# Kernel tuning notes

Measured on AMD Instinct MI355X. Metric: run time of the kernel, lower is better.

The kernel has to match this reference:

```python
import jax, jax.numpy as jnp
import numpy as np

EPS = 1e-12  # F.normalize default eps


def setup_inputs() -> dict:
    key = jax.random.key(0)
    ks = jax.random.split(key, 8)
    b, c, h, w = 8, 192, 128, 128
    s = 0.02
    return {
        "x_in": jax.random.normal(ks[0], (b, c, h, w), dtype=jnp.float32),
        "w_split": jax.random.normal(ks[1], (c, c), dtype=jnp.float32) * s,
        "w_q": jax.random.normal(ks[2], (c, c), dtype=jnp.float32) * s,
        "w_k": jax.random.normal(ks[3], (c, c), dtype=jnp.float32) * s,
        "w_v": jax.random.normal(ks[4], (c, c), dtype=jnp.float32) * s,
        "w_proj": jax.random.normal(ks[5], (c, c), dtype=jnp.float32) * s,
        "b_proj": jax.random.normal(ks[6], (c,), dtype=jnp.float32) * s,
        "w_out": jax.random.normal(ks[7], (c, c), dtype=jnp.float32) * s,
    }


def _l2norm(x):
    # F.normalize(p=2, dim=-1): x / max(||x||, eps)
    n = jnp.sqrt(jnp.sum(x * x, axis=-1, keepdims=True))
    return x / jnp.maximum(n, EPS)


def reference(x_in, w_split, w_q, w_k, w_v, w_proj, b_proj, w_out):
    b, c, h, w = x_in.shape
    # conv_split0: 1x1 conv, no bias -> channel matmul
    x = jnp.einsum('oc,bchw->bohw', w_split, x_in)
    # [b,h,w,c] -> [b,hw,c]
    x = x.transpose(0, 2, 3, 1).reshape(b, h * w, c)
    # Linear: y = x @ W^T
    q = jnp.einsum('bnc,oc->bon', x, w_q)  # [b,c,hw] (already transposed)
    k = jnp.einsum('bnc,oc->bon', x, w_k)
    v = jnp.einsum('bnc,oc->bon', x, w_v)
    q = _l2norm(q)
    k = _l2norm(k)
    attn = jax.nn.softmax(jnp.einsum('bcn,bdn->bcd', k, q), axis=-1)  # [b,c,c]
    y = jnp.einsum('bcd,bdn->bcn', attn, v)  # [b,c,hw]
    y = y.transpose(0, 2, 1)  # [b,hw,c]
    out = jnp.einsum('bnc,oc->bno', y, w_proj) + b_proj
    out = out.reshape(b, h, w, c).transpose(0, 3, 1, 2)  # [b,c,h,w]
    out = jnp.einsum('oc,bchw->bohw', w_out, out)
    return out
```

## Files before the change

### kernel.cpp

```cpp
#include <hip/hip_runtime.h>


static constexpr int B_ = 8;
static constexpr int C_ = 192;
static constexpr int N_ = 16384;
static constexpr int CC2 = C_ * C_;
static constexpr int NCHUNK = 32;

using u16x8 = __attribute__((ext_vector_type(8))) unsigned short;
using bf16x8 = __attribute__((ext_vector_type(8))) __bf16;
using f32x4 = __attribute__((ext_vector_type(4))) float;
using uint32x4 = __attribute__((ext_vector_type(4))) unsigned int;

__device__ __forceinline__ unsigned short f2bf(float f) {
  unsigned int u = __builtin_bit_cast(unsigned int, f);
  u += 0x7FFFu + ((u >> 16) & 1u);
  return (unsigned short)(u >> 16);
}

__device__ __forceinline__ unsigned int pkbf(float lo, float hi) {
  unsigned short a = __builtin_bit_cast(unsigned short, (__bf16)lo);
  unsigned short b = __builtin_bit_cast(unsigned short, (__bf16)hi);
  return (unsigned int)a | ((unsigned int)b << 16);
}

__device__ __forceinline__ float f4get(const float4& v, int e) {
  return (e == 0) ? v.x : (e == 1) ? v.y : (e == 2) ? v.z : v.w;
}

__device__ __forceinline__ f32x4 mfma16(u16x8 a, u16x8 b, f32x4 c) {
  return __builtin_amdgcn_mfma_f32_16x16x32_bf16(
      __builtin_bit_cast(bf16x8, a), __builtin_bit_cast(bf16x8, b), c, 0, 0, 0);
}

__global__ void fold_kernel(const float* __restrict__ wsplit, const float* __restrict__ wq,
                            const float* __restrict__ wk, const float* __restrict__ wv,
                            const float* __restrict__ wproj, const float* __restrict__ bproj,
                            const float* __restrict__ wout,
                            float* __restrict__ Wq, float* __restrict__ WqT,
                            float* __restrict__ Wk, float* __restrict__ Wv,
                            float* __restrict__ Wo2, float* __restrict__ bias2) {
  int idx = blockIdx.x * 256 + threadIdx.x;
  if (idx < C_) {
    float s = 0.f;
    for (int c = 0; c < C_; ++c) s += wout[idx * C_ + c] * bproj[c];
    bias2[idx] = s;
  }
  if (idx >= 4 * CC2) return;
  int which = idx / CC2;
  int rem = idx % CC2;
  int o = rem / C_, c = rem % C_;
  const float* A = (which == 0) ? wq : (which == 1) ? wk : (which == 2) ? wv : wout;
  const float* Bm = (which == 3) ? wproj : wsplit;
  float s = 0.f;
  for (int e = 0; e < C_; ++e) s += A[o * C_ + e] * Bm[e * C_ + c];
  if (which == 0) { Wq[rem] = s; WqT[c * C_ + o] = s; }
  else if (which == 1) Wk[rem] = s;
  else if (which == 2) Wv[rem] = s;
  else Wo2[rem] = s;
}

template <bool ATOMIC>
__global__ __launch_bounds__(384) void gram3_kernel(const float* __restrict__ xin,
                                                    float* __restrict__ dst) {
  const int b = blockIdx.z, half = blockIdx.y, ch = blockIdx.x;
  const int k0 = ch * 512;
  __shared__ unsigned short Xs[2][C_][72];
  const int tid = threadIdx.x;
  const int wv = tid >> 6;
  const int lane = tid & 63;
  const int ln = lane & 15, mq = lane >> 4;
  const int arow0 = half * 96 + wv * 16;
  const int cbase = tid >> 4;
  const int k4 = tid & 15;
  const float* xb = xin + (size_t)b * C_ * N_;

  f32x4 acc[12];
#pragma unroll
  for (int j = 0; j < 12; ++j) acc[j] = (f32x4)0.0f;

  float4 ld[8];
  auto load_stage = [&](int kbase) {
#pragma unroll
    for (int j = 0; j < 8; ++j)
      ld[j] = *(const float4*)(xb + (size_t)(j * 24 + cbase) * N_ + kbase + k4 * 4);
  };
  auto write_stage = [&](int buf) {
#pragma unroll
    for (int j = 0; j < 8; ++j) {
      unsigned int lo = (unsigned)f2bf(ld[j].x) | ((unsigned)f2bf(ld[j].y) << 16);
      unsigned int hi = (unsigned)f2bf(ld[j].z) | ((unsigned)f2bf(ld[j].w) << 16);
      uint2 pk; pk.x = lo; pk.y = hi;
      *(uint2*)&Xs[buf][j * 24 + cbase][k4 * 4] = pk;
    }
  };

  load_stage(k0);
  write_stage(0);
  __syncthreads();
  for (int s = 0; s < 8; ++s) {
    if (s < 7) load_stage(k0 + (s + 1) * 64);
    const int cb = s & 1;
#pragma unroll
    for (int ks = 0; ks < 2; ++ks) {
      const int kk = ks * 32 + mq * 8;
      u16x8 a0 = *(const u16x8*)&Xs[cb][arow0 + ln][kk];
#pragma unroll
      for (int ct = 0; ct < 12; ++ct) {
        u16x8 bf = *(const u16x8*)&Xs[cb][ct * 16 + ln][kk];
        acc[ct] = mfma16(a0, bf, acc[ct]);
      }
    }
    if (s < 7) {
      write_stage(cb ^ 1);
      __syncthreads();
    }
  }
  float* out = ATOMIC ? dst + (size_t)b * CC2
                      : dst + ((size_t)b * NCHUNK + ch) * CC2;
#pragma unroll
  for (int ct = 0; ct < 12; ++ct)
#pragma unroll
    for (int r = 0; r < 4; ++r) {
      int row = arow0 + mq * 4 + r;
      int col = ct * 16 + ln;
      if (ATOMIC) atomicAdd(&out[row * C_ + col], acc[ct][r]);
      else out[row * C_ + col] = acc[ct][r];
    }
}

__global__ void gsum_kernel(const float* __restrict__ P, float* __restrict__ G) {
  const int j = (blockIdx.x * 256 + threadIdx.x) * 4;
  const int b = blockIdx.y;
  const float* base = P + (size_t)b * NCHUNK * CC2 + j;
  float4 s = {0.f, 0.f, 0.f, 0.f};
#pragma unroll
  for (int ch = 0; ch < NCHUNK; ++ch) {
    float4 v = *(const float4*)(base + (size_t)ch * CC2);
    s.x += v.x; s.y += v.y; s.z += v.z; s.w += v.w;
  }
  *(float4*)(G + (size_t)b * CC2 + j) = s;
}

__global__ __launch_bounds__(192) void tkqn_kernel(const float* __restrict__ Wk,
                                                   const float* __restrict__ Wq,
                                                   const float* __restrict__ G,
                                                   float* __restrict__ Tk,
                                                   float* __restrict__ qn) {
  const int b = blockIdx.y, d = blockIdx.x, t = threadIdx.x;
  const float* Gb = G + (size_t)b * CC2;
  float sk = 0.f, sq = 0.f;
  for (int c = 0; c < C_; ++c) {
    float g = Gb[c * C_ + t];
    sk += Wk[d * C_ + c] * g;
    sq += Wq[d * C_ + c] * g;
  }
  Tk[((size_t)b * C_ + d) * C_ + t] = sk;
  float val = sq * Wq[d * C_ + t];
  __shared__ float red[256];
  red[t] = val;
  if (t < 64) red[192 + t] = 0.f;
  __syncthreads();
  for (int st = 128; st > 0; st >>= 1) {
    if (t < st) red[t] += red[t + st];
    __syncthreads();
  }
  if (t == 0) qn[b * C_ + d] = fmaxf(sqrtf(fmaxf(red[0], 0.f)), 1e-12f);
}

__global__ __launch_bounds__(192) void attn_av_kernel(const float* __restrict__ Tk,
                                                      const float* __restrict__ WqT,
                                                      const float* __restrict__ Wk,
                                                      const float* __restrict__ Wv,
                                                      const float* __restrict__ qn,
                                                      float* __restrict__ Tv) {
  const int b = blockIdx.y, cc = blockIdx.x, t = threadIdx.x;
  __shared__ float tkrow[C_];
  __shared__ float arow[C_];
  __shared__ float red[256];
  tkrow[t] = Tk[((size_t)b * C_ + cc) * C_ + t];
  red[t] = tkrow[t] * Wk[cc * C_ + t];
  if (t < 64) red[192 + t] = 0.f;
  __syncthreads();
  for (int st = 128; st > 0; st >>= 1) {
    if (t < st) red[t] += red[t + st];
    __syncthreads();
  }
  float knv = fmaxf(sqrtf(fmaxf(red[0], 0.f)), 1e-12f);
  __syncthreads();
  float s = 0.f;
  for (int c = 0; c < C_; ++c) s += tkrow[c] * WqT[c * C_ + t];
  float lg = s / (knv * qn[b * C_ + t]);
  red[t] = lg;
  if (t < 64) red[192 + t] = -1e30f;
  __syncthreads();
  for (int st = 128; st > 0; st >>= 1) {
    if (t < st) red[t] = fmaxf(red[t], red[t + st]);
    __syncthreads();
  }
  float mx = red[0];
  __syncthreads();
  float e = expf(lg - mx);
  red[t] = e;
  if (t < 64) red[192 + t] = 0.f;
  __syncthreads();
  for (int st = 128; st > 0; st >>= 1) {
    if (t < st) red[t] += red[t + st];
    __syncthreads();
  }
  float a = e / red[0];
  arow[t] = a;
  __syncthreads();
  float sv = 0.f;
  for (int c = 0; c < C_; ++c) sv += arow[c] * Wv[c * C_ + t];
  Tv[((size_t)b * C_ + cc) * C_ + t] = sv;
}

__global__ void m_kernel(const float* __restrict__ Wo2, const float* __restrict__ Tv,
                         float* __restrict__ Mout) {
  int idx = blockIdx.x * 256 + threadIdx.x;
  if (idx >= B_ * CC2) return;
  int b = idx / CC2;
  int rc = idx % CC2;
  int i = rc / C_, j = rc % C_;
  float s = 0.f;
  for (int c = 0; c < C_; ++c) s += Wo2[i * C_ + c] * Tv[((size_t)b * C_ + c) * C_ + j];
  Mout[idx] = s;
}

__global__ __launch_bounds__(384, 4) void final3_kernel(const float* __restrict__ xin,
                                                        const float* __restrict__ Mw,
                                                        const float* __restrict__ bias2,
                                                        float* __restrict__ out) {
  const int b = blockIdx.y;
  const int p0 = blockIdx.x * 64;
  __shared__ __align__(16) unsigned short Ts[64 * 192];
  const int tid = threadIdx.x;
  const int wv = tid >> 6;
  const int lane = tid & 63;
  const int ln = lane & 15, mq = lane >> 4;
  const float* Mb = Mw + (size_t)b * CC2;

  const int c0 = (tid >> 3) * 4;
  const int pq = tid & 7;
  const float* xsrc = xin + ((size_t)b * C_ + c0) * N_ + p0 + pq * 4;

  float4 ldA[4], ldB[4];
#pragma unroll
  for (int l = 0; l < 4; ++l) ldA[l] = *(const float4*)(xsrc + (size_t)l * N_);

  u16x8 afr[6][2];
  float bo[2][4];
#pragma unroll
  for (int i = 0; i < 2; ++i) {
    int row = 32 * wv + 16 * i + ln;
#pragma unroll
    for (int kc = 0; kc < 6; ++kc) {
      const float* src = Mb + row * C_ + kc * 32 + mq * 8;
      float4 u0 = *(const float4*)(src);
      float4 u1 = *(const float4*)(src + 4);
      uint32x4 w;
      w[0] = pkbf(u0.x, u0.y); w[1] = pkbf(u0.z, u0.w);
      w[2] = pkbf(u1.x, u1.y); w[3] = pkbf(u1.z, u1.w);
      afr[kc][i] = __builtin_bit_cast(u16x8, w);
    }
#pragma unroll
    for (int r = 0; r < 4; ++r) bo[i][r] = bias2[32 * wv + 16 * i + mq * 4 + r];
  }

  auto stage_write = [&](const float4* ld, int sbase) {
#pragma unroll
    for (int e = 0; e < 4; ++e) {
      int p = sbase + pq * 4 + e;
      int idx = p * 192 + ((((c0 >> 3) ^ ((p >> 1) & 7)) << 3) | (c0 & 7));
      uint2 pk;
      pk.x = pkbf(f4get(ld[0], e), f4get(ld[1], e));
      pk.y = pkbf(f4get(ld[2], e), f4get(ld[3], e));
      *(uint2*)&Ts[idx] = pk;
    }
  };

  auto compute = [&](int pt) {
    const int p = pt * 16 + ln;
    const int pkey = (p >> 1) & 7;
    f32x4 acc0 = (f32x4)0.0f, acc1 = (f32x4)0.0f;
#pragma unroll
    for (int kc = 0; kc < 6; ++kc) {
      u16x8 bf = *(const u16x8*)&Ts[p * 192 + (((kc * 4 + mq) ^ pkey) << 3)];
      acc0 = mfma16(afr[kc][0], bf, acc0);
      acc1 = mfma16(afr[kc][1], bf, acc1);
    }
    const int pp = p0 + p;
#pragma unroll
    for (int r = 0; r < 4; ++r) {
      int row0 = 32 * wv + mq * 4 + r;
      out[((size_t)b * C_ + row0) * N_ + pp] = acc0[r] + bo[0][r];
      out[((size_t)b * C_ + row0 + 16) * N_ + pp] = acc1[r] + bo[1][r];
    }
  };

  stage_write(ldA, 0);
  __syncthreads();
#pragma unroll
  for (int l = 0; l < 4; ++l) ldB[l] = *(const float4*)(xsrc + 32 + (size_t)l * N_);
  compute(0);
  compute(1);
  stage_write(ldB, 32);
  __syncthreads();
  compute(2);
  compute(3);
}

extern "C" void kernel_launch(void* const* d_in, const int* in_sizes, int n_in,
                              void* d_out, int out_size, void* d_ws, size_t ws_size,
                              hipStream_t stream) {
  const float* xin    = (const float*)d_in[0];
  const float* wsplit = (const float*)d_in[1];
  const float* wq     = (const float*)d_in[2];
  const float* wk     = (const float*)d_in[3];
  const float* wv     = (const float*)d_in[4];
  const float* wproj  = (const float*)d_in[5];
  const float* bproj  = (const float*)d_in[6];
  const float* wout   = (const float*)d_in[7];
  float* out = (float*)d_out;

  float* ws = (float*)d_ws;
  float* G     = ws;
  float* Wq    = G + (size_t)B_ * CC2;
  float* WqT   = Wq + CC2;
  float* Wk    = WqT + CC2;
  float* Wv    = Wk + CC2;
  float* Wo2   = Wv + CC2;
  float* bias2 = Wo2 + CC2;
  float* Tk    = bias2 + 256;
  float* Tv    = Tk + (size_t)B_ * CC2;
  float* Mw    = Tv + (size_t)B_ * CC2;
  float* qn    = Mw + (size_t)B_ * CC2;
  float* P     = qn + 256 * B_;

  size_t base_floats = (size_t)(P - ws);
  size_t need_bytes = (base_floats + (size_t)B_ * NCHUNK * CC2) * sizeof(float);
  bool use_partials = ws_size >= need_bytes;

  fold_kernel<<<(4 * CC2 + 255) / 256, 256, 0, stream>>>(
      wsplit, wq, wk, wv, wproj, bproj, wout, Wq, WqT, Wk, Wv, Wo2, bias2);
  if (use_partials) {
    gram3_kernel<false><<<dim3(NCHUNK, 2, B_), 384, 0, stream>>>(xin, P);
    gsum_kernel<<<dim3(CC2 / 1024, B_), 256, 0, stream>>>(P, G);
  } else {
    hipMemsetAsync(G, 0, (size_t)B_ * CC2 * sizeof(float), stream);
    gram3_kernel<true><<<dim3(NCHUNK, 2, B_), 384, 0, stream>>>(xin, G);
  }
  tkqn_kernel<<<dim3(C_, B_), 192, 0, stream>>>(Wk, Wq, G, Tk, qn);
  attn_av_kernel<<<dim3(C_, B_), 192, 0, stream>>>(Tk, WqT, Wk, Wv, qn, Tv);
  m_kernel<<<(B_ * CC2 + 255) / 256, 256, 0, stream>>>(Wo2, Tv, Mw);
  final3_kernel<<<dim3(N_ / 64, B_), 384, 0, stream>>>(xin, Mw, bias2, out);
}
```

Before: 314.9 us.

## Fuse gram-reduction, attention and M-matrix kernels into one cooperative grid-synced kernel

Replaces the partial-sum, Tk/qn, attention/Tv and M-matrix kernels with one cooperative kernel of 512 blocks that separates phases with grid.sync. This removes three kernel launches and the gaps between them. In exchange each block processes three rows serially and grid-wide barriers are added. The bf16 packing in the gram kernel also switches to the native conversion.

```diff
diff --git a/kernel.cpp b/kernel.cpp
--- a/kernel.cpp
+++ b/kernel.cpp
@@ -1,4 +1,7 @@
 #include <hip/hip_runtime.h>
+#include <hip/hip_cooperative_groups.h>
+
+namespace cg = cooperative_groups;
 
 
 static constexpr int B_ = 8;
@@ -88,9 +91,9 @@
   auto write_stage = [&](int buf) {
 #pragma unroll
     for (int j = 0; j < 8; ++j) {
-      unsigned int lo = (unsigned)f2bf(ld[j].x) | ((unsigned)f2bf(ld[j].y) << 16);
-      unsigned int hi = (unsigned)f2bf(ld[j].z) | ((unsigned)f2bf(ld[j].w) << 16);
-      uint2 pk; pk.x = lo; pk.y = hi;
+      uint2 pk;
+      pk.x = pkbf(ld[j].x, ld[j].y);
+      pk.y = pkbf(ld[j].z, ld[j].w);
       *(uint2*)&Xs[buf][j * 24 + cbase][k4 * 4] = pk;
     }
   };
@@ -129,103 +132,122 @@
     }
 }
 
-__global__ void gsum_kernel(const float* __restrict__ P, float* __restrict__ G) {
-  const int j = (blockIdx.x * 256 + threadIdx.x) * 4;
-  const int b = blockIdx.y;
-  const float* base = P + (size_t)b * NCHUNK * CC2 + j;
-  float4 s = {0.f, 0.f, 0.f, 0.f};
-#pragma unroll
-  for (int ch = 0; ch < NCHUNK; ++ch) {
-    float4 v = *(const float4*)(base + (size_t)ch * CC2);
-    s.x += v.x; s.y += v.y; s.z += v.z; s.w += v.w;
-  }
-  *(float4*)(G + (size_t)b * CC2 + j) = s;
-}
-
-__global__ __launch_bounds__(192) void tkqn_kernel(const float* __restrict__ Wk,
-                                                   const float* __restrict__ Wq,
-                                                   const float* __restrict__ G,
-                                                   float* __restrict__ Tk,
-                                                   float* __restrict__ qn) {
-  const int b = blockIdx.y, d = blockIdx.x, t = threadIdx.x;
-  const float* Gb = G + (size_t)b * CC2;
-  float sk = 0.f, sq = 0.f;
-  for (int c = 0; c < C_; ++c) {
-    float g = Gb[c * C_ + t];
-    sk += Wk[d * C_ + c] * g;
-    sq += Wq[d * C_ + c] * g;
-  }
-  Tk[((size_t)b * C_ + d) * C_ + t] = sk;
-  float val = sq * Wq[d * C_ + t];
-  __shared__ float red[256];
-  red[t] = val;
-  if (t < 64) red[192 + t] = 0.f;
-  __syncthreads();
-  for (int st = 128; st > 0; st >>= 1) {
-    if (t < st) red[t] += red[t + st];
-    __syncthreads();
-  }
-  if (t == 0) qn[b * C_ + d] = fmaxf(sqrtf(fmaxf(red[0], 0.f)), 1e-12f);
-}
-
-__global__ __launch_bounds__(192) void attn_av_kernel(const float* __restrict__ Tk,
-                                                      const float* __restrict__ WqT,
-                                                      const float* __restrict__ Wk,
-                                                      const float* __restrict__ Wv,
-                                                      const float* __restrict__ qn,
-                                                      float* __restrict__ Tv) {
-  const int b = blockIdx.y, cc = blockIdx.x, t = threadIdx.x;
+template <bool SUMP>
+__global__ __launch_bounds__(256) void middle_kernel(
+    const float* __restrict__ P, float* __restrict__ G,
+    const float* __restrict__ Wk, const float* __restrict__ Wq,
+    const float* __restrict__ WqT, const float* __restrict__ Wv,
+    const float* __restrict__ Wo2, float* __restrict__ Tk,
+    float* __restrict__ qn, float* __restrict__ Tv, float* __restrict__ Mw) {
+  cg::grid_group grid = cg::this_grid();
+  const int blk = blockIdx.x;
+  const int t = threadIdx.x;
   __shared__ float tkrow[C_];
   __shared__ float arow[C_];
   __shared__ float red[256];
-  tkrow[t] = Tk[((size_t)b * C_ + cc) * C_ + t];
-  red[t] = tkrow[t] * Wk[cc * C_ + t];
-  if (t < 64) red[192 + t] = 0.f;
-  __syncthreads();
-  for (int st = 128; st > 0; st >>= 1) {
-    if (t < st) red[t] += red[t + st];
-    __syncthreads();
-  }
-  float knv = fmaxf(sqrtf(fmaxf(red[0], 0.f)), 1e-12f);
-  __syncthreads();
-  float s = 0.f;
-  for (int c = 0; c < C_; ++c) s += tkrow[c] * WqT[c * C_ + t];
-  float lg = s / (knv * qn[b * C_ + t]);
-  red[t] = lg;
-  if (t < 64) red[192 + t] = -1e30f;
-  __syncthreads();
-  for (int st = 128; st > 0; st >>= 1) {
-    if (t < st) red[t] = fmaxf(red[t], red[t + st]);
-    __syncthreads();
-  }
-  float mx = red[0];
-  __syncthreads();
-  float e = expf(lg - mx);
-  red[t] = e;
-  if (t < 64) red[192 + t] = 0.f;
-  __syncthreads();
-  for (int st = 128; st > 0; st >>= 1) {
-    if (t < st) red[t] += red[t + st];
-    __syncthreads();
-  }
-  float a = e / red[0];
-  arow[t] = a;
-  __syncthreads();
-  float sv = 0.f;
-  for (int c = 0; c < C_; ++c) sv += arow[c] * Wv[c * C_ + t];
-  Tv[((size_t)b * C_ + cc) * C_ + t] = sv;
-}
-
-__global__ void m_kernel(const float* __restrict__ Wo2, const float* __restrict__ Tv,
-                         float* __restrict__ Mout) {
-  int idx = blockIdx.x * 256 + threadIdx.x;
-  if (idx >= B_ * CC2) return;
-  int b = idx / CC2;
-  int rc = idx % CC2;
-  int i = rc / C_, j = rc % C_;
-  float s = 0.f;
-  for (int c = 0; c < C_; ++c) s += Wo2[i * C_ + c] * Tv[((size_t)b * C_ + c) * C_ + j];
-  Mout[idx] = s;
+
+  if (SUMP) {
+    for (int idx4 = blk * 256 + t; idx4 < B_ * CC2 / 4; idx4 += 512 * 256) {
+      int b = idx4 / (CC2 / 4);
+      int jj = idx4 % (CC2 / 4);
+      const float* base = P + (size_t)b * NCHUNK * CC2 + jj * 4;
+      float4 s = {0.f, 0.f, 0.f, 0.f};
+#pragma unroll
+      for (int ch = 0; ch < NCHUNK; ++ch) {
+        float4 v = *(const float4*)(base + (size_t)ch * CC2);
+        s.x += v.x; s.y += v.y; s.z += v.z; s.w += v.w;
+      }
+      *(float4*)(G + (size_t)b * CC2 + jj * 4) = s;
+    }
+    __threadfence();
+    grid.sync();
+  }
+
+  for (int r = 0; r < 3; ++r) {
+    const int task = blk + 512 * r;
+    const int b = task / C_, d = task % C_;
+    const float* Gb = G + (size_t)b * CC2;
+    float sq = 0.f;
+    if (t < C_) {
+      float sk = 0.f;
+      for (int c = 0; c < C_; ++c) {
+        float g = Gb[c * C_ + t];
+        sk += Wk[d * C_ + c] * g;
+        sq += Wq[d * C_ + c] * g;
+      }
+      Tk[((size_t)b * C_ + d) * C_ + t] = sk;
+    }
+    red[t] = (t < C_) ? sq * Wq[d * C_ + t] : 0.f;
+    __syncthreads();
+    for (int st = 128; st > 0; st >>= 1) {
+      if (t < st) red[t] += red[t + st];
+      __syncthreads();
+    }
+    if (t == 0) qn[b * C_ + d] = fmaxf(sqrtf(fmaxf(red[0], 0.f)), 1e-12f);
+    __syncthreads();
+  }
+  __threadfence();
+  grid.sync();
+
+  for (int r = 0; r < 3; ++r) {
+    const int task = blk + 512 * r;
+    const int b = task / C_, cc = task % C_;
+    float tkv = 0.f;
+    if (t < C_) {
+      tkv = Tk[((size_t)b * C_ + cc) * C_ + t];
+      tkrow[t] = tkv;
+    }
+    red[t] = (t < C_) ? tkv * Wk[cc * C_ + t] : 0.f;
+    __syncthreads();
+    for (int st = 128; st > 0; st >>= 1) {
+      if (t < st) red[t] += red[t + st];
+      __syncthreads();
+    }
+    float knv = fmaxf(sqrtf(fmaxf(red[0], 0.f)), 1e-12f);
+    __syncthreads();
+    float lg = -1e30f;
+    if (t < C_) {
+      float s = 0.f;
+      for (int c = 0; c < C_; ++c) s += tkrow[c] * WqT[c * C_ + t];
+      lg = s / (knv * qn[b * C_ + t]);
+    }
+    red[t] = lg;
+    __syncthreads();
+    for (int st = 128; st > 0; st >>= 1) {
+      if (t < st) red[t] = fmaxf(red[t], red[t + st]);
+      __syncthreads();
+    }
+    float mx = red[0];
+    __syncthreads();
+    float e = (t < C_) ? expf(lg - mx) : 0.f;
+    red[t] = e;
+    __syncthreads();
+    for (int st = 128; st > 0; st >>= 1) {
+      if (t < st) red[t] += red[t + st];
+      __syncthreads();
+    }
+    float a = e / red[0];
+    __syncthreads();
+    if (t < C_) arow[t] = a;
+    __syncthreads();
+    if (t < C_) {
+      float sv = 0.f;
+      for (int c = 0; c < C_; ++c) sv += arow[c] * Wv[c * C_ + t];
+      Tv[((size_t)b * C_ + cc) * C_ + t] = sv;
+    }
+    __syncthreads();
+  }
+  __threadfence();
+  grid.sync();
+
+  for (int idx = blk * 256 + t; idx < B_ * CC2; idx += 512 * 256) {
+    int b = idx / CC2;
+    int rc = idx % CC2;
+    int i = rc / C_, j = rc % C_;
+    float s = 0.f;
+    for (int c = 0; c < C_; ++c) s += Wo2[i * C_ + c] * Tv[((size_t)b * C_ + c) * C_ + j];
+    Mw[idx] = s;
+  }
 }
 
 __global__ __launch_bounds__(384, 4) void final3_kernel(const float* __restrict__ xin,
@@ -344,15 +366,25 @@
 
   fold_kernel<<<(4 * CC2 + 255) / 256, 256, 0, stream>>>(
       wsplit, wq, wk, wv, wproj, bproj, wout, Wq, WqT, Wk, Wv, Wo2, bias2);
+
   if (use_partials) {
     gram3_kernel<false><<<dim3(NCHUNK, 2, B_), 384, 0, stream>>>(xin, P);
-    gsum_kernel<<<dim3(CC2 / 1024, B_), 256, 0, stream>>>(P, G);
+    const float* Pc = P;
+    void* args[] = {(void*)&Pc, (void*)&G, (void*)&Wk, (void*)&Wq, (void*)&WqT,
+                    (void*)&Wv, (void*)&Wo2, (void*)&Tk, (void*)&qn, (void*)&Tv,
+                    (void*)&Mw};
+    hipLaunchCooperativeKernel((const void*)middle_kernel<true>, dim3(512), dim3(256),
+                               args, 0, stream);
   } else {
     hipMemsetAsync(G, 0, (size_t)B_ * CC2 * sizeof(float), stream);
     gram3_kernel<true><<<dim3(NCHUNK, 2, B_), 384, 0, stream>>>(xin, G);
-  }
-  tkqn_kernel<<<dim3(C_, B_), 192, 0, stream>>>(Wk, Wq, G, Tk, qn);
-  attn_av_kernel<<<dim3(C_, B_), 192, 0, stream>>>(Tk, WqT, Wk, Wv, qn, Tv);
-  m_kernel<<<(B_ * CC2 + 255) / 256, 256, 0, stream>>>(Wo2, Tv, Mw);
+    const float* Pc = G;
+    void* args[] = {(void*)&Pc, (void*)&G, (void*)&Wk, (void*)&Wq, (void*)&WqT,
+                    (void*)&Wv, (void*)&Wo2, (void*)&Tk, (void*)&qn, (void*)&Tv,
+                    (void*)&Mw};
+    hipLaunchCooperativeKernel((const void*)middle_kernel<false>, dim3(512), dim3(256),
+                               args, 0, stream);
+  }
+
   final3_kernel<<<dim3(N_ / 64, B_), 384, 0, stream>>>(xin, Mw, bias2, out);
 }
```

Measured after the change: 650.9 us. 2.07x slower.

## Rewrite small 192x192 attention-chain kernels with bf16 MFMA tiles

Applied to the files above, without the earlier changes.

Replaces the scalar per-row tkqn, attn_av and m kernels with MFMA-based tile kernels. Tk/norm, logits+softmax+AV, and the Wo2·Tv product each run as 16x16x32 bf16 MFMA GEMMs, with softmax reductions done via lane shuffles instead of shared-memory tree reductions. Tv is stored transposed in bf16 to feed the final GEMM directly. This adds bf16 rounding to small intermediate matrices, and the grids are now very small (24–48 blocks), which may underuse the GPU.

```diff
diff --git a/kernel.cpp b/kernel.cpp
--- a/kernel.cpp
+++ b/kernel.cpp
@@ -24,6 +24,15 @@
   return (unsigned int)a | ((unsigned int)b << 16);
 }
 
+__device__ __forceinline__ u16x8 ld8bf(const float* p) {
+  float4 u0 = *(const float4*)p;
+  float4 u1 = *(const float4*)(p + 4);
+  uint32x4 w;
+  w[0] = pkbf(u0.x, u0.y); w[1] = pkbf(u0.z, u0.w);
+  w[2] = pkbf(u1.x, u1.y); w[3] = pkbf(u1.z, u1.w);
+  return __builtin_bit_cast(u16x8, w);
+}
+
 __device__ __forceinline__ float f4get(const float4& v, int e) {
   return (e == 0) ? v.x : (e == 1) ? v.y : (e == 2) ? v.z : v.w;
 }
@@ -37,7 +46,7 @@
                             const float* __restrict__ wk, const float* __restrict__ wv,
                             const float* __restrict__ wproj, const float* __restrict__ bproj,
                             const float* __restrict__ wout,
-                            float* __restrict__ Wq, float* __restrict__ WqT,
+                            float* __restrict__ Wq, float* __restrict__ WvT,
                             float* __restrict__ Wk, float* __restrict__ Wv,
                             float* __restrict__ Wo2, float* __restrict__ bias2) {
   int idx = blockIdx.x * 256 + threadIdx.x;
@@ -54,9 +63,9 @@
   const float* Bm = (which == 3) ? wproj : wsplit;
   float s = 0.f;
   for (int e = 0; e < C_; ++e) s += A[o * C_ + e] * Bm[e * C_ + c];
-  if (which == 0) { Wq[rem] = s; WqT[c * C_ + o] = s; }
+  if (which == 0) Wq[rem] = s;
   else if (which == 1) Wk[rem] = s;
-  else if (which == 2) Wv[rem] = s;
+  else if (which == 2) { Wv[rem] = s; WvT[c * C_ + o] = s; }
   else Wo2[rem] = s;
 }
 
@@ -88,9 +97,9 @@
   auto write_stage = [&](int buf) {
 #pragma unroll
     for (int j = 0; j < 8; ++j) {
-      unsigned int lo = (unsigned)f2bf(ld[j].x) | ((unsigned)f2bf(ld[j].y) << 16);
-      unsigned int hi = (unsigned)f2bf(ld[j].z) | ((unsigned)f2bf(ld[j].w) << 16);
-      uint2 pk; pk.x = lo; pk.y = hi;
+      uint2 pk;
+      pk.x = pkbf(ld[j].x, ld[j].y);
+      pk.y = pkbf(ld[j].z, ld[j].w);
       *(uint2*)&Xs[buf][j * 24 + cbase][k4 * 4] = pk;
     }
   };
@@ -142,90 +151,175 @@
   *(float4*)(G + (size_t)b * CC2 + j) = s;
 }
 
-__global__ __launch_bounds__(192) void tkqn_kernel(const float* __restrict__ Wk,
-                                                   const float* __restrict__ Wq,
-                                                   const float* __restrict__ G,
-                                                   float* __restrict__ Tk,
-                                                   float* __restrict__ qn) {
-  const int b = blockIdx.y, d = blockIdx.x, t = threadIdx.x;
+__global__ __launch_bounds__(256) void tkqn2_kernel(
+    const float* __restrict__ Wk, const float* __restrict__ Wq,
+    const float* __restrict__ G, float* __restrict__ Tk,
+    float* __restrict__ kn, float* __restrict__ qn) {
+  const int b = blockIdx.y;
+  const int row0 = blockIdx.x * 64;
+  const int tid = threadIdx.x;
+  const int w = tid >> 6, lane = tid & 63;
+  const int ln = lane & 15, mq = lane >> 4;
+  const int rbase = row0 + w * 16;
+  const bool isq = rbase >= C_;
+  const float* W2 = isq ? Wq : Wk;
+  const int rloc = isq ? rbase - C_ : rbase;
   const float* Gb = G + (size_t)b * CC2;
-  float sk = 0.f, sq = 0.f;
-  for (int c = 0; c < C_; ++c) {
-    float g = Gb[c * C_ + t];
-    sk += Wk[d * C_ + c] * g;
-    sq += Wq[d * C_ + c] * g;
-  }
-  Tk[((size_t)b * C_ + d) * C_ + t] = sk;
-  float val = sq * Wq[d * C_ + t];
-  __shared__ float red[256];
-  red[t] = val;
-  if (t < 64) red[192 + t] = 0.f;
+
+  f32x4 acc[12];
+#pragma unroll
+  for (int j = 0; j < 12; ++j) acc[j] = (f32x4)0.0f;
+
+  for (int kc = 0; kc < 6; ++kc) {
+    u16x8 a = ld8bf(W2 + (size_t)(rloc + ln) * C_ + kc * 32 + mq * 8);
+#pragma unroll
+    for (int ct = 0; ct < 12; ++ct) {
+      u16x8 g = ld8bf(Gb + (size_t)(ct * 16 + ln) * C_ + kc * 32 + mq * 8);
+      acc[ct] = mfma16(a, g, acc[ct]);
+    }
+  }
+  const float* wr = W2 + (size_t)(rloc + mq * 4) * C_;
+  float nrm[4] = {0.f, 0.f, 0.f, 0.f};
+#pragma unroll
+  for (int ct = 0; ct < 12; ++ct)
+#pragma unroll
+    for (int r = 0; r < 4; ++r)
+      nrm[r] += acc[ct][r] * wr[r * C_ + ct * 16 + ln];
+#pragma unroll
+  for (int m = 1; m < 16; m <<= 1)
+#pragma unroll
+    for (int r = 0; r < 4; ++r) nrm[r] += __shfl_xor(nrm[r], m);
+  if (ln == 0) {
+#pragma unroll
+    for (int r = 0; r < 4; ++r) {
+      float v = fmaxf(sqrtf(fmaxf(nrm[r], 0.f)), 1e-12f);
+      int row = rbase + mq * 4 + r;
+      if (row < C_) kn[b * 256 + row] = v;
+      else qn[b * 256 + row - C_] = v;
+    }
+  }
+  if (!isq) {
+#pragma unroll
+    for (int ct = 0; ct < 12; ++ct)
+#pragma unroll
+      for (int r = 0; r < 4; ++r)
+        Tk[((size_t)b * C_ + rbase + mq * 4 + r) * C_ + ct * 16 + ln] = acc[ct][r];
+  }
+}
+
+__global__ __launch_bounds__(256) void attn2_kernel(
+    const float* __restrict__ Tk, const float* __restrict__ Wq,
+    const float* __restrict__ WvT, const float* __restrict__ kn,
+    const float* __restrict__ qn, unsigned short* __restrict__ Tvt) {
+  __shared__ unsigned short As[64 * 200];
+  const int b = blockIdx.y;
+  const int row0 = blockIdx.x * 64;
+  const int tid = threadIdx.x;
+  const int w = tid >> 6, lane = tid & 63;
+  const int ln = lane & 15, mq = lane >> 4;
+  const int rbase = row0 + w * 16;
+
+  f32x4 acc[12];
+#pragma unroll
+  for (int j = 0; j < 12; ++j) acc[j] = (f32x4)0.0f;
+  for (int kc = 0; kc < 6; ++kc) {
+    u16x8 a = ld8bf(Tk + ((size_t)b * C_ + rbase + ln) * C_ + kc * 32 + mq * 8);
+#pragma unroll
+    for (int ct = 0; ct < 12; ++ct) {
+      u16x8 q = ld8bf(Wq + (size_t)(ct * 16 + ln) * C_ + kc * 32 + mq * 8);
+      acc[ct] = mfma16(a, q, acc[ct]);
+    }
+  }
+  float rkn[4], rqn[12];
+#pragma unroll
+  for (int r = 0; r < 4; ++r) rkn[r] = kn[b * 256 + rbase + mq * 4 + r];
+#pragma unroll
+  for (int ct = 0; ct < 12; ++ct) rqn[ct] = qn[b * 256 + ct * 16 + ln];
+
+  float mx[4] = {-1e30f, -1e30f, -1e30f, -1e30f};
+#pragma unroll
+  for (int ct = 0; ct < 12; ++ct)
+#pragma unroll
+    for (int r = 0; r < 4; ++r) {
+      float l = acc[ct][r] / (rkn[r] * rqn[ct]);
+      acc[ct][r] = l;
+      mx[r] = fmaxf(mx[r], l);
+    }
+#pragma unroll
+  for (int m = 1; m < 16; m <<= 1)
+#pragma unroll
+    for (int r = 0; r < 4; ++r) mx[r] = fmaxf(mx[r], __shfl_xor(mx[r], m));
+  float sm[4] = {0.f, 0.f, 0.f, 0.f};
+#pragma unroll
+  for (int ct = 0; ct < 12; ++ct)
+#pragma unroll
+    for (int r = 0; r < 4; ++r) {
+      float e = expf(acc[ct][r] - mx[r]);
+      acc[ct][r] = e;
+      sm[r] += e;
+    }
+#pragma unroll
+  for (int m = 1; m < 16; m <<= 1)
+#pragma unroll
+    for (int r = 0; r < 4; ++r) sm[r] += __shfl_xor(sm[r], m);
+  float inv[4];
+#pragma unroll
+  for (int r = 0; r < 4; ++r) inv[r] = 1.f / sm[r];
+#pragma unroll
+  for (int ct = 0; ct < 12; ++ct)
+#pragma unroll
+    for (int r = 0; r < 4; ++r) {
+      int lrow = w * 16 + mq * 4 + r;
+      As[lrow * 200 + ct * 16 + ln] = f2bf(acc[ct][r] * inv[r]);
+    }
   __syncthreads();
-  for (int st = 128; st > 0; st >>= 1) {
-    if (t < st) red[t] += red[t + st];
-    __syncthreads();
-  }
-  if (t == 0) qn[b * C_ + d] = fmaxf(sqrtf(fmaxf(red[0], 0.f)), 1e-12f);
-}
-
-__global__ __launch_bounds__(192) void attn_av_kernel(const float* __restrict__ Tk,
-                                                      const float* __restrict__ WqT,
-                                                      const float* __restrict__ Wk,
-                                                      const float* __restrict__ Wv,
-                                                      const float* __restrict__ qn,
-                                                      float* __restrict__ Tv) {
-  const int b = blockIdx.y, cc = blockIdx.x, t = threadIdx.x;
-  __shared__ float tkrow[C_];
-  __shared__ float arow[C_];
-  __shared__ float red[256];
-  tkrow[t] = Tk[((size_t)b * C_ + cc) * C_ + t];
-  red[t] = tkrow[t] * Wk[cc * C_ + t];
-  if (t < 64) red[192 + t] = 0.f;
-  __syncthreads();
-  for (int st = 128; st > 0; st >>= 1) {
-    if (t < st) red[t] += red[t + st];
-    __syncthreads();
-  }
-  float knv = fmaxf(sqrtf(fmaxf(red[0], 0.f)), 1e-12f);
-  __syncthreads();
-  float s = 0.f;
-  for (int c = 0; c < C_; ++c) s += tkrow[c] * WqT[c * C_ + t];
-  float lg = s / (knv * qn[b * C_ + t]);
-  red[t] = lg;
-  if (t < 64) red[192 + t] = -1e30f;
-  __syncthreads();
-  for (int st = 128; st > 0; st >>= 1) {
-    if (t < st) red[t] = fmaxf(red[t], red[t + st]);
-    __syncthreads();
-  }
-  float mx = red[0];
-  __syncthreads();
-  float e = expf(lg - mx);
-  red[t] = e;
-  if (t < 64) red[192 + t] = 0.f;
-  __syncthreads();
-  for (int st = 128; st > 0; st >>= 1) {
-    if (t < st) red[t] += red[t + st];
-    __syncthreads();
-  }
-  float a = e / red[0];
-  arow[t] = a;
-  __syncthreads();
-  float sv = 0.f;
-  for (int c = 0; c < C_; ++c) sv += arow[c] * Wv[c * C_ + t];
-  Tv[((size_t)b * C_ + cc) * C_ + t] = sv;
-}
-
-__global__ void m_kernel(const float* __restrict__ Wo2, const float* __restrict__ Tv,
-                         float* __restrict__ Mout) {
-  int idx = blockIdx.x * 256 + threadIdx.x;
-  if (idx >= B_ * CC2) return;
-  int b = idx / CC2;
-  int rc = idx % CC2;
-  int i = rc / C_, j = rc % C_;
-  float s = 0.f;
-  for (int c = 0; c < C_; ++c) s += Wo2[i * C_ + c] * Tv[((size_t)b * C_ + c) * C_ + j];
-  Mout[idx] = s;
+
+  f32x4 tv[12];
+#pragma unroll
+  for (int j = 0; j < 12; ++j) tv[j] = (f32x4)0.0f;
+  for (int kc = 0; kc < 6; ++kc) {
+    u16x8 a2 = *(const u16x8*)&As[(w * 16 + ln) * 200 + kc * 32 + mq * 8];
+#pragma unroll
+    for (int ct = 0; ct < 12; ++ct) {
+      u16x8 q = ld8bf(WvT + (size_t)(ct * 16 + ln) * C_ + kc * 32 + mq * 8);
+      tv[ct] = mfma16(a2, q, tv[ct]);
+    }
+  }
+#pragma unroll
+  for (int ct = 0; ct < 12; ++ct) {
+    uint2 pk;
+    pk.x = pkbf(tv[ct][0], tv[ct][1]);
+    pk.y = pkbf(tv[ct][2], tv[ct][3]);
+    *(uint2*)&Tvt[((size_t)b * C_ + ct * 16 + ln) * C_ + row0 + w * 16 + mq * 4] = pk;
+  }
+}
+
+__global__ __launch_bounds__(256) void m2_kernel(
+    const float* __restrict__ Wo2, const unsigned short* __restrict__ Tvt,
+    float* __restrict__ Mw) {
+  const int b = blockIdx.y;
+  const int row0 = blockIdx.x * 64;
+  const int tid = threadIdx.x;
+  const int w = tid >> 6, lane = tid & 63;
+  const int ln = lane & 15, mq = lane >> 4;
+  const int rbase = row0 + w * 16;
+
+  f32x4 acc[12];
+#pragma unroll
+  for (int j = 0; j < 12; ++j) acc[j] = (f32x4)0.0f;
+  for (int kc = 0; kc < 6; ++kc) {
+    u16x8 a = ld8bf(Wo2 + (size_t)(rbase + ln) * C_ + kc * 32 + mq * 8);
+#pragma unroll
+    for (int ct = 0; ct < 12; ++ct) {
+      u16x8 q = *(const u16x8*)&Tvt[((size_t)b * C_ + ct * 16 + ln) * C_ + kc * 32 + mq * 8];
+      acc[ct] = mfma16(a, q, acc[ct]);
+    }
+  }
+#pragma unroll
+  for (int ct = 0; ct < 12; ++ct)
+#pragma unroll
+    for (int r = 0; r < 4; ++r)
+      Mw[(size_t)b * CC2 + (rbase + mq * 4 + r) * C_ + ct * 16 + ln] = acc[ct][r];
 }
 
 __global__ __launch_bounds__(384, 4) void final3_kernel(const float* __restrict__ xin,
@@ -327,23 +421,24 @@
   float* ws = (float*)d_ws;
   float* G     = ws;
   float* Wq    = G + (size_t)B_ * CC2;
-  float* WqT   = Wq + CC2;
-  float* Wk    = WqT + CC2;
+  float* WvT   = Wq + CC2;
+  float* Wk    = WvT + CC2;
   float* Wv    = Wk + CC2;
   float* Wo2   = Wv + CC2;
   float* bias2 = Wo2 + CC2;
   float* Tk    = bias2 + 256;
-  float* Tv    = Tk + (size_t)B_ * CC2;
-  float* Mw    = Tv + (size_t)B_ * CC2;
+  float* Tvt_f = Tk + (size_t)B_ * CC2;
+  float* Mw    = Tvt_f + (size_t)B_ * CC2;
   float* qn    = Mw + (size_t)B_ * CC2;
-  float* P     = qn + 256 * B_;
+  float* kn    = qn + 256 * B_;
+  float* P     = kn + 256 * B_;
 
   size_t base_floats = (size_t)(P - ws);
   size_t need_bytes = (base_floats + (size_t)B_ * NCHUNK * CC2) * sizeof(float);
   bool use_partials = ws_size >= need_bytes;
 
   fold_kernel<<<(4 * CC2 + 255) / 256, 256, 0, stream>>>(
-      wsplit, wq, wk, wv, wproj, bproj, wout, Wq, WqT, Wk, Wv, Wo2, bias2);
+      wsplit, wq, wk, wv, wproj, bproj, wout, Wq, WvT, Wk, Wv, Wo2, bias2);
   if (use_partials) {
     gram3_kernel<false><<<dim3(NCHUNK, 2, B_), 384, 0, stream>>>(xin, P);
     gsum_kernel<<<dim3(CC2 / 1024, B_), 256, 0, stream>>>(P, G);
@@ -351,8 +446,9 @@
     hipMemsetAsync(G, 0, (size_t)B_ * CC2 * sizeof(float), stream);
     gram3_kernel<true><<<dim3(NCHUNK, 2, B_), 384, 0, stream>>>(xin, G);
   }
-  tkqn_kernel<<<dim3(C_, B_), 192, 0, stream>>>(Wk, Wq, G, Tk, qn);
-  attn_av_kernel<<<dim3(C_, B_), 192, 0, stream>>>(Tk, WqT, Wk, Wv, qn, Tv);
-  m_kernel<<<(B_ * CC2 + 255) / 256, 256, 0, stream>>>(Wo2, Tv, Mw);
+  tkqn2_kernel<<<dim3(6, B_), 256, 0, stream>>>(Wk, Wq, G, Tk, kn, qn);
+  attn2_kernel<<<dim3(3, B_), 256, 0, stream>>>(Tk, Wq, WvT, kn, qn,
+                                                (unsigned short*)Tvt_f);
+  m2_kernel<<<dim3(3, B_), 256, 0, stream>>>(Wo2, (const unsigned short*)Tvt_f, Mw);
   final3_kernel<<<dim3(N_ / 64, B_), 384, 0, stream>>>(xin, Mw, bias2, out);
 }
```

Measured after the change: 366.7 us. 1.16x slower.
